# Performance work log

Hardware: AMD Instinct MI355X
Metric: run time of the kernel (lower is better)

Reference implementation:

```python
import jax, jax.numpy as jnp
import numpy as np
from jax import lax

VOCAB, D, H, K = 20000, 100, 100, 3
N_U, N_I, R, S, E = 256, 256, 8, 52, 20000


def _text_processor(reviews, emb_table, conv_w, conv_b):
    # reviews: [B,R,S] int -> c: [B,R,S',H]
    B, Rr, Ss = reviews.shape
    embs = emb_table[reviews]                              # [B,R,S,D]
    x = embs.reshape(B * Rr, 1, Ss, D)                     # NCHW
    c = lax.conv_general_dilated(x, conv_w, (1, 1), 'VALID',
                                 dimension_numbers=('NCHW', 'OIHW', 'NCHW'))
    c = jax.nn.relu(c + conv_b[None, :, None, None])       # [B*R,H,S',1]
    Sp = Ss - K + 1
    c = c[..., 0].transpose(0, 2, 1).reshape(B, Rr, Sp, H) # [B,R,S',H]
    return c


def _branch(reviews, emb_table, conv_w, conv_b, fc_w_w, fc_w_b, fc_w2_w, fc_w2_b):
    c = _text_processor(reviews, emb_table, conv_w, conv_b)
    rho = jax.nn.sigmoid(c @ fc_w_w.T + fc_w_b)            # [B,R,S',1]
    z = rho + lax.stop_gradient(jnp.round(rho) - rho)      # straight-through round
    z = z[..., 0]                                          # [B,R,S']
    P = jnp.max(c, axis=-2) @ fc_w2_w.T + fc_w2_b          # [B,R,D]
    return P, z


def reference(user_reviews, item_reviews, uid, iid, emb_table, conv_w, conv_b,
              fc_w_w, fc_w_b, fc_w2_w, fc_w2_b, h_r_w, h_c_w,
              user_bias, item_bias, global_bias):
    P_u, z_u = _branch(user_reviews, emb_table, conv_w, conv_b, fc_w_w, fc_w_b, fc_w2_w, fc_w2_b)
    P_i, z_i = _branch(item_reviews, emb_table, conv_w, conv_b, fc_w_w, fc_w_b, fc_w2_w, fc_w2_b)
    Pu, Pi = P_u[uid], P_i[iid]                            # edge gathers [E,R,D]
    zu, zi = z_u[uid], z_i[iid]                            # [E,R,S']
    s_uv = jnp.einsum('eud,evd->euv', Pu, Pi)              # per-edge review similarity [E,R,R]
    rho_u = jax.nn.sigmoid(s_uv.sum(-1))                   # [E,R]
    rho_v = jax.nn.sigmoid(s_uv.sum(-2))                   # [E,R]
    gamma_u_r = jnp.einsum('ers,er->es', zu, rho_u)        # [E,S']
    gamma_v_r = jnp.einsum('ers,er->es', zi, rho_v)
    pred_r = (jnp.concatenate([gamma_u_r, gamma_v_r], -1) @ h_r_w.T
              + user_bias[uid] + item_bias[iid] + global_bias)  # [E,1]
    gamma_u_c = jnp.einsum('er,erd->ed', rho_u, Pu)        # [E,D]
    gamma_v_c = jnp.einsum('er,erd->ed', rho_v, Pi)
    pred_c = jnp.concatenate([gamma_u_c, gamma_v_c], -1) @ h_c_w.T  # [E,1]
    return pred_r, pred_c, z_u, z_i


def setup_inputs() -> dict:
    key = jax.random.key(0)
    ks = jax.random.split(key, 12)
    return {
        'user_reviews': jax.random.randint(ks[0], (N_U, R, S), 0, VOCAB, dtype=jnp.int32),
        'item_reviews': jax.random.randint(ks[1], (N_I, R, S), 0, VOCAB, dtype=jnp.int32),
        'uid': jax.random.randint(ks[2], (E,), 0, N_U, dtype=jnp.int32),
        'iid': jax.random.randint(ks[3], (E,), 0, N_I, dtype=jnp.int32),
        'emb_table': jax.random.normal(ks[4], (VOCAB, D), jnp.float32) * 0.1,
        'conv_w': jax.random.normal(ks[5], (H, 1, K, D), jnp.float32) * 0.05,
        'conv_b': jnp.zeros((H,), jnp.float32),
        'fc_w_w': jax.random.normal(ks[6], (1, H), jnp.float32) * 0.1,
        'fc_w_b': jnp.zeros((1,), jnp.float32),
        'fc_w2_w': jax.random.normal(ks[7], (D, H), jnp.float32) * 0.1,
        'fc_w2_b': jnp.zeros((D,), jnp.float32),
        'h_r_w': jax.random.normal(ks[8], (1, 2 * (S - K + 1)), jnp.float32) * 0.1,
        'h_c_w': jax.random.normal(ks[9], (1, 2 * D), jnp.float32) * 0.1,
        'user_bias': jnp.zeros((N_U, 1), jnp.float32),
        'item_bias': jnp.zeros((N_I, 1), jnp.float32),
        'global_bias': jnp.zeros((1,), jnp.float32),
    }
```

## Files before the change

### kernel.cpp

```cpp
#include <hip/hip_runtime.h>
#include <math.h>


typedef __attribute__((ext_vector_type(8))) short short8;
typedef __attribute__((ext_vector_type(4))) float f32x4;

__device__ __forceinline__ float sigmoidf_(float x) { return 1.f / (1.f + expf(-x)); }
__device__ __forceinline__ ushort f2b(float f) {
    union { float f; unsigned int i; } c; c.f = f;
    unsigned int x = c.i;
    return (ushort)((x + 0x7fffu + ((x >> 16) & 1u)) >> 16);
}
__device__ __forceinline__ unsigned int pack_hl(float x) {
    union { float f; unsigned int i; } c; c.f = x;
    unsigned int hi = c.i & 0xFFFF0000u;
    union { float f; unsigned int i; } h; h.i = hi;
    return hi | (unsigned int)f2b(x - h.f);
}

#define Z_MARGIN 2e-3f
#define FLAG_CAP 204800

__global__ void k_prep(const float* __restrict__ conv_w, const float* __restrict__ fc_w2_w,
                       float* __restrict__ Wt, float* __restrict__ fc2t,
                       float* __restrict__ Psum, ushort* __restrict__ wpack,
                       int* __restrict__ flag_cnt) {
    int idx = blockIdx.x * 256 + threadIdx.x;
    if (idx < 30000) {
        int kk = idx / 100, h = idx - kk * 100;
        Wt[idx] = conv_w[h * 300 + kk];
    } else if (idx < 40000) {
        int j = idx - 30000;
        int h = j / 100, dd = j - h * 100;
        fc2t[j] = fc_w2_w[dd * 100 + h];
    } else if (idx < 91200) {
        Psum[idx - 40000] = 0.f;
    } else if (idx < 127040) {
        int j = idx - 91200;
        int frag = j >> 9, within = j & 511;
        int l = within >> 3, jj = within & 7;
        int kt = frag / 7, nt = frag % 7;
        int kk = kt * 32 + ((l >> 4) << 3) + jj;
        int h  = nt * 16 + (l & 15);
        ushort v = 0;
        if (kk < 300 && h < 100) v = f2b(conv_w[h * 300 + kk]);
        wpack[j] = v;
    } else if (idx == 127040) {
        *flag_cnt = 0;
    }
}

__global__ __launch_bounds__(256, 4)
void k_branch(const int* __restrict__ u_rev, const int* __restrict__ i_rev,
              const float* __restrict__ emb, const ushort* __restrict__ wpack,
              const float* __restrict__ conv_b, const float* __restrict__ fc_w_w,
              const float* __restrict__ fc_w_b, const float* __restrict__ fc_w2_b,
              const float* __restrict__ fc2t, const float* __restrict__ h_r_w,
              const float* __restrict__ h_c_w,
              float* __restrict__ Pbuf, float* __restrict__ Psum,
              float* __restrict__ zdot, float* __restrict__ Pdot,
              float* __restrict__ z_out, int* __restrict__ flag_cnt,
              int* __restrict__ flag_list) {
    __shared__ __align__(16) char smem[36816];
    unsigned int* xw   = (unsigned int*)smem;
    ushort* wbuf  = (ushort*)(smem + 26624);
    int*    s_tok = (int*)(smem + 33792);
    float*  s_vmax= (float*)(smem + 34000);
    float*  s_maxf= (float*)(smem + 35600);
    float*  s_z   = (float*)(smem + 36000);
    float*  s_lg  = (float*)(smem + 36208);
    float*  s_P   = (float*)(smem + 36416);

    const int tid = threadIdx.x, lane = tid & 63, w = tid >> 6;
    const int gi = blockIdx.x;
    const int branch = gi >> 11, inst = gi & 2047;

    const uint4* wp4 = (const uint4*)wpack;
    uint4* wbuf4 = (uint4*)wbuf;
    uint4 st0 = wp4[tid];
    uint4 st1; if (tid < 192) st1 = wp4[256 + tid];

    const int* rev = branch ? i_rev : u_rev;
    if (tid < 52) s_tok[tid] = rev[inst * 52 + tid];
    __syncthreads();

    {
        const float4* emb4 = (const float4*)emb;
        float4 v[6];
#pragma unroll
        for (int k = 0; k < 6; k++) {
            int idx = tid + (k << 8);
            if (idx < 1300) {
                int s = idx / 25, c = idx - s * 25;
                v[k] = emb4[s_tok[s] * 25 + c];
            }
        }
#pragma unroll
        for (int k = 0; k < 6; k++) {
            int idx = tid + (k << 8);
            if (idx < 1300) {
                uint4 o;
                o.x = pack_hl(v[k].x); o.y = pack_hl(v[k].y);
                o.z = pack_hl(v[k].z); o.w = pack_hl(v[k].w);
                *(uint4*)(xw + idx * 4) = o;
            }
        }
        for (int idx = 1300 + tid; idx < 1664; idx += 256) {
            uint4 z; z.x = 0u; z.y = 0u; z.z = 0u; z.w = 0u;
            *(uint4*)(xw + idx * 4) = z;
        }
    }

    wbuf4[tid] = st0;
    if (tid < 192) wbuf4[256 + tid] = st1;
    st0 = wp4[448 + tid];
    if (tid < 192) st1 = wp4[448 + 256 + tid];
    __syncthreads();

    f32x4 acc[7];
#pragma unroll
    for (int nt = 0; nt < 7; nt++) acc[nt] = (f32x4){0.f, 0.f, 0.f, 0.f};

    const int col = lane & 15, quad = lane >> 4, q8 = quad << 3;
    const int mt = w;

    for (int kt = 0; kt < 10; kt++) {
        {
            int e0 = (mt * 16 + col) * 100 + kt * 32 + q8;
            uint4 xa = *(const uint4*)(xw + e0);
            uint4 xb = *(const uint4*)(xw + e0 + 4);
            union AU { short8 s8; uint4 u; } ah, al;
            ah.u.x = (xa.x >> 16) | (xa.y & 0xFFFF0000u);
            ah.u.y = (xa.z >> 16) | (xa.w & 0xFFFF0000u);
            ah.u.z = (xb.x >> 16) | (xb.y & 0xFFFF0000u);
            ah.u.w = (xb.z >> 16) | (xb.w & 0xFFFF0000u);
            al.u.x = (xa.x & 0xFFFFu) | (xa.y << 16);
            al.u.y = (xa.z & 0xFFFFu) | (xa.w << 16);
            al.u.z = (xb.x & 0xFFFFu) | (xb.y << 16);
            al.u.w = (xb.z & 0xFFFFu) | (xb.w << 16);
#pragma unroll
            for (int nt = 0; nt < 7; nt++) {
                union BU { short8 s8; uint4 u4; } b;
                b.u4 = wbuf4[nt * 64 + lane];
                acc[nt] = __builtin_amdgcn_mfma_f32_16x16x32_bf16(al.s8, b.s8, acc[nt], 0, 0, 0);
                acc[nt] = __builtin_amdgcn_mfma_f32_16x16x32_bf16(ah.s8, b.s8, acc[nt], 0, 0, 0);
            }
        }
        __syncthreads();
        if (kt < 9) {
            wbuf4[tid] = st0;
            if (tid < 192) wbuf4[256 + tid] = st1;
            if (kt < 8) {
                st0 = wp4[(kt + 2) * 448 + tid];
                if (tid < 192) st1 = wp4[(kt + 2) * 448 + 256 + tid];
            }
            __syncthreads();
        }
    }

    float cb[7], fw[7], vmax[7];
#pragma unroll
    for (int nt = 0; nt < 7; nt++) {
        int h = nt * 16 + col;
        cb[nt] = (h < 100) ? conv_b[h] : 0.f;
        fw[nt] = (h < 100) ? fc_w_w[h] : 0.f;
        vmax[nt] = 0.f;
    }
    const float fcb = fc_w_b[0];

#pragma unroll
    for (int j = 0; j < 4; j++) {
        int p = mt * 16 + quad * 4 + j;
        bool pv = p < 50;
        float part = 0.f;
#pragma unroll
        for (int nt = 0; nt < 7; nt++) {
            float c = acc[nt][j] + cb[nt];
            c = c > 0.f ? c : 0.f;
            part += c * fw[nt];
            if (pv) vmax[nt] = fmaxf(vmax[nt], c);
        }
        part += __shfl_xor(part, 1, 64);
        part += __shfl_xor(part, 2, 64);
        part += __shfl_xor(part, 4, 64);
        part += __shfl_xor(part, 8, 64);
        if (pv && col == 0) {
            float logit = part + fcb;
            float z = rintf(sigmoidf_(logit));
            s_z[p] = z;
            s_lg[p] = logit;
            z_out[branch * 102400 + inst * 50 + p] = z;
        }
    }

#pragma unroll
    for (int nt = 0; nt < 7; nt++) {
        float m = vmax[nt];
        m = fmaxf(m, __shfl_xor(m, 16, 64));
        m = fmaxf(m, __shfl_xor(m, 32, 64));
        int h = nt * 16 + col;
        if (quad == 0 && h < 100) s_vmax[w * 100 + h] = m;
    }
    __syncthreads();

    if (tid < 100) {
        float mx = fmaxf(fmaxf(s_vmax[tid], s_vmax[100 + tid]),
                         fmaxf(s_vmax[200 + tid], s_vmax[300 + tid]));
        s_maxf[tid] = mx;
    }
    __syncthreads();

    if (tid < 100) {
        float a = fc_w2_b[tid];
        for (int h0 = 0; h0 < 100; h0 += 10) {
            float wv[10], mxv[10];
#pragma unroll
            for (int t = 0; t < 10; t++) {
                wv[t] = fc2t[(h0 + t) * 100 + tid];
                mxv[t] = s_maxf[h0 + t];
            }
#pragma unroll
            for (int t = 0; t < 10; t++) a += mxv[t] * wv[t];
        }
        Pbuf[gi * 100 + tid] = a;
        s_P[tid] = a;
        atomicAdd(&Psum[(branch * 256 + (inst >> 3)) * 100 + tid], a);
    }
    __syncthreads();

    if (w == 0) {
        float v = (lane < 50) ? s_z[lane] * h_r_w[branch * 50 + lane] : 0.f;
        for (int s = 1; s < 64; s <<= 1) v += __shfl_xor(v, s, 64);
        if (lane == 0) zdot[gi] = v;
    } else if (w == 1) {
        float u = 0.f;
        if (lane < 50) u = s_P[lane] * h_c_w[branch * 100 + lane]
                         + s_P[lane + 50] * h_c_w[branch * 100 + lane + 50];
        for (int s = 1; s < 64; s <<= 1) u += __shfl_xor(u, s, 64);
        if (lane == 0) Pdot[gi] = u;
    } else if (w == 2) {
        float lg = 1e9f;
        if (lane < 50) lg = s_lg[lane];
        unsigned long long mb = __ballot(fabsf(lg) < Z_MARGIN);
        int cnt = __popcll(mb);
        int base = 0;
        if (lane == 0 && cnt) base = atomicAdd(flag_cnt, cnt);
        base = __shfl(base, 0, 64);
        if (fabsf(lg) < Z_MARGIN) {
            int rank = __popcll(mb & ((1ull << lane) - 1ull));
            int k = base + rank;
            if (k < FLAG_CAP) flag_list[k] = gi * 50 + lane;
        }
    }
}

__launch_bounds__(256)
__global__ void k_refine(const int* __restrict__ u_rev, const int* __restrict__ i_rev,
                         const float* __restrict__ emb, const float* __restrict__ Wt,
                         const float* __restrict__ conv_b, const float* __restrict__ fc_w_w,
                         const float* __restrict__ fc_w_b, const float* __restrict__ h_r_w,
                         const int* __restrict__ flag_cnt, const int* __restrict__ flag_list,
                         float* __restrict__ z_out, float* __restrict__ zdot) {
    int n = *flag_cnt; if (n > FLAG_CAP) n = FLAG_CAP;
    const int lane = threadIdx.x & 63;
    const int wid = (blockIdx.x * 256 + threadIdx.x) >> 6;
    const int nw = gridDim.x * 4;
    const bool hv = lane < 50;
    const float cb0 = hv ? conv_b[lane] : 0.f;
    const float cb1 = hv ? conv_b[lane + 50] : 0.f;
    const float fw0 = hv ? fc_w_w[lane] : 0.f;
    const float fw1 = hv ? fc_w_w[lane + 50] : 0.f;
    const float fcb = fc_w_b[0];

    for (int e0 = wid * 4; e0 < n; e0 += nw * 4) {
        int gi[4], pos[4];
        bool iv[4];
        float xr[4][5];
#pragma unroll
        for (int m = 0; m < 4; m++) {
            int e = e0 + m;
            iv[m] = e < n;
            int code = iv[m] ? flag_list[e] : 0;
            gi[m] = code / 50; pos[m] = code - gi[m] * 50;
            const int* rev = (gi[m] >> 11) ? i_rev : u_rev;
            int tb = (gi[m] & 2047) * 52 + pos[m];
            int t0 = rev[tb], t1 = rev[tb + 1], t2 = rev[tb + 2];
#pragma unroll
            for (int s = 0; s < 5; s++) {
                int k = s * 64 + lane;
                float v = 0.f;
                if (k < 300) {
                    int r = k / 100, dd = k - r * 100;
                    int t = (r == 0) ? t0 : ((r == 1) ? t1 : t2);
                    v = emb[t * 100 + dd];
                }
                xr[m][s] = v;
            }
        }
        float c0[4], c1[4];
#pragma unroll
        for (int m = 0; m < 4; m++) { c0[m] = cb0; c1[m] = cb1; }
#pragma unroll
        for (int s = 0; s < 5; s++) {
            const int dmax = (s < 4) ? 64 : 44;
#pragma unroll 4
            for (int d2 = 0; d2 < dmax; d2++) {
                int d = s * 64 + d2;
                float w0 = hv ? Wt[d * 100 + lane] : 0.f;
                float w1 = hv ? Wt[d * 100 + lane + 50] : 0.f;
#pragma unroll
                for (int m = 0; m < 4; m++) {
                    float x = __shfl(xr[m][s], d2, 64);
                    c0[m] += x * w0;
                    c1[m] += x * w1;
                }
            }
        }
#pragma unroll
        for (int m = 0; m < 4; m++) {
            float v = fmaxf(c0[m], 0.f) * fw0 + fmaxf(c1[m], 0.f) * fw1;
            for (int s = 1; s < 64; s <<= 1) v += __shfl_xor(v, s, 64);
            if (lane == 0 && iv[m]) {
                int branch = gi[m] >> 11, inst = gi[m] & 2047;
                float z = rintf(sigmoidf_(v + fcb));
                float old = z_out[branch * 102400 + inst * 50 + pos[m]];
                if (z != old) {
                    z_out[branch * 102400 + inst * 50 + pos[m]] = z;
                    atomicAdd(&zdot[gi[m]], (z - old) * h_r_w[branch * 50 + pos[m]]);
                }
            }
        }
    }
}

__launch_bounds__(256)
__global__ void k_edge(const int* __restrict__ uid, const int* __restrict__ iid,
                       const float* __restrict__ Pbuf, const float* __restrict__ Psum,
                       const float* __restrict__ zdot, const float* __restrict__ Pdot,
                       const float* __restrict__ user_bias, const float* __restrict__ item_bias,
                       const float* __restrict__ global_bias, float* __restrict__ out) {
    int wave = threadIdx.x >> 6, lane = threadIdx.x & 63;
    int e = blockIdx.x * 4 + wave;
    int u = uid[e], i = iid[e];
    int g = lane >> 2, q = lane & 3;
    const float4* prow4; const float4* psum4; float wr, wc;
    if (g < 8) {
        prow4 = (const float4*)(Pbuf + (u * 8 + g) * 100);
        psum4 = (const float4*)(Psum + 25600 + i * 100);
        wr = zdot[u * 8 + g]; wc = Pdot[u * 8 + g];
    } else {
        prow4 = (const float4*)(Pbuf + (2048 + i * 8 + (g - 8)) * 100);
        psum4 = (const float4*)(Psum + u * 100);
        wr = zdot[2048 + i * 8 + (g - 8)]; wc = Pdot[2048 + i * 8 + (g - 8)];
    }
    float part = 0.f;
#pragma unroll
    for (int t = 0; t < 7; t++) {
        int c = q + 4 * t;
        if (c < 25) {
            float4 a = prow4[c], b = psum4[c];
            part += a.x * b.x + a.y * b.y + a.z * b.z + a.w * b.w;
        }
    }
    part += __shfl_xor(part, 1, 64);
    part += __shfl_xor(part, 2, 64);
    float sg = sigmoidf_(part);
    float cr = (q == 0) ? sg * wr : 0.f;
    float cc = (q == 0) ? sg * wc : 0.f;
    for (int s = 4; s < 64; s <<= 1) { cr += __shfl_xor(cr, s, 64); cc += __shfl_xor(cc, s, 64); }
    if (lane == 0) {
        out[e] = cr + user_bias[u] + item_bias[i] + global_bias[0];
        out[20000 + e] = cc;
    }
}

extern "C" void kernel_launch(void* const* d_in, const int* in_sizes, int n_in,
                              void* d_out, int out_size, void* d_ws, size_t ws_size,
                              hipStream_t stream) {
    const int*   u_rev    = (const int*)d_in[0];
    const int*   i_rev    = (const int*)d_in[1];
    const int*   uid      = (const int*)d_in[2];
    const int*   iid      = (const int*)d_in[3];
    const float* emb      = (const float*)d_in[4];
    const float* conv_w   = (const float*)d_in[5];
    const float* conv_b   = (const float*)d_in[6];
    const float* fc_w_w   = (const float*)d_in[7];
    const float* fc_w_b   = (const float*)d_in[8];
    const float* fc_w2_w  = (const float*)d_in[9];
    const float* fc_w2_b  = (const float*)d_in[10];
    const float* h_r_w    = (const float*)d_in[11];
    const float* h_c_w    = (const float*)d_in[12];
    const float* user_b   = (const float*)d_in[13];
    const float* item_b   = (const float*)d_in[14];
    const float* global_b = (const float*)d_in[15];
    float* out = (float*)d_out;

    float*  ws    = (float*)d_ws;
    float*  Pbuf  = ws;
    float*  Psum  = ws + 409600;
    float*  zdotb = ws + 460800;
    float*  Pdotb = ws + 464896;
    float*  Wt    = ws + 468992;
    float*  fc2t  = ws + 498992;
    ushort* wpack = (ushort*)(ws + 508992);
    int*    flagc = (int*)(ws + 526912);
    int*    flist = (int*)(ws + 526916);

    hipLaunchKernelGGL(k_prep, dim3(497), dim3(256), 0, stream,
                       conv_w, fc_w2_w, Wt, fc2t, Psum, wpack, flagc);
    hipLaunchKernelGGL(k_branch, dim3(4096), dim3(256), 0, stream,
                       u_rev, i_rev, emb, wpack, conv_b, fc_w_w, fc_w_b,
                       fc_w2_b, fc2t, h_r_w, h_c_w,
                       Pbuf, Psum, zdotb, Pdotb, out + 40000, flagc, flist);
    hipLaunchKernelGGL(k_refine, dim3(512), dim3(256), 0, stream,
                       u_rev, i_rev, emb, Wt, conv_b, fc_w_w, fc_w_b, h_r_w,
                       flagc, flist, out + 40000, zdotb);
    hipLaunchKernelGGL(k_edge, dim3(5000), dim3(256), 0, stream,
                       uid, iid, Pbuf, Psum, zdotb, Pdotb,
                       user_b, item_b, global_b, out);
}
```

Measured before the change: 211.6 us.

## Switch conv GEMM to single fp16 MFMA and precompute per-pair similarity matrix

Result: slower. 224.9 us (+6.3%).

```diff
diff --git a/kernel.cpp b/kernel.cpp
--- a/kernel.cpp
+++ b/kernel.cpp
@@ -1,30 +1,27 @@
 #include <hip/hip_runtime.h>
+#include <hip/hip_fp16.h>
 #include <math.h>
 
 
-typedef __attribute__((ext_vector_type(8))) short short8;
+typedef __attribute__((ext_vector_type(8))) _Float16 half8;
 typedef __attribute__((ext_vector_type(4))) float f32x4;
 
 __device__ __forceinline__ float sigmoidf_(float x) { return 1.f / (1.f + expf(-x)); }
-__device__ __forceinline__ ushort f2b(float f) {
-    union { float f; unsigned int i; } c; c.f = f;
-    unsigned int x = c.i;
-    return (ushort)((x + 0x7fffu + ((x >> 16) & 1u)) >> 16);
-}
-__device__ __forceinline__ unsigned int pack_hl(float x) {
-    union { float f; unsigned int i; } c; c.f = x;
-    unsigned int hi = c.i & 0xFFFF0000u;
-    union { float f; unsigned int i; } h; h.i = hi;
-    return hi | (unsigned int)f2b(x - h.f);
-}
-
-#define Z_MARGIN 2e-3f
+__device__ __forceinline__ ushort f2h(float x) {
+    union { __half h; ushort u; } t; t.h = __float2half(x); return t.u;
+}
+__device__ __forceinline__ float h2f(ushort u) {
+    union { __half h; ushort u; } t; t.u = u; return __half2float(t.h);
+}
+
+#define Z_MARGIN 4e-4f
 #define FLAG_CAP 204800
 
 __global__ void k_prep(const float* __restrict__ conv_w, const float* __restrict__ fc_w2_w,
+                       const float* __restrict__ emb,
                        float* __restrict__ Wt, float* __restrict__ fc2t,
                        float* __restrict__ Psum, ushort* __restrict__ wpack,
-                       int* __restrict__ flag_cnt) {
+                       int* __restrict__ flag_cnt, ushort* __restrict__ emb16) {
     int idx = blockIdx.x * 256 + threadIdx.x;
     if (idx < 30000) {
         int kk = idx / 100, h = idx - kk * 100;
@@ -42,17 +39,18 @@
         int kt = frag / 7, nt = frag % 7;
         int kk = kt * 32 + ((l >> 4) << 3) + jj;
         int h  = nt * 16 + (l & 15);
-        ushort v = 0;
-        if (kk < 300 && h < 100) v = f2b(conv_w[h * 300 + kk]);
-        wpack[j] = v;
+        wpack[j] = (kk < 300 && h < 100) ? f2h(conv_w[h * 300 + kk]) : (ushort)0;
     } else if (idx == 127040) {
         *flag_cnt = 0;
-    }
-}
-
-__global__ __launch_bounds__(256, 4)
+    } else {
+        int j = idx - 127041;
+        if (j < 2000000) emb16[j] = f2h(emb[j]);
+    }
+}
+
+__global__ __launch_bounds__(256, 6)
 void k_branch(const int* __restrict__ u_rev, const int* __restrict__ i_rev,
-              const float* __restrict__ emb, const ushort* __restrict__ wpack,
+              const ushort* __restrict__ emb16, const ushort* __restrict__ wpack,
               const float* __restrict__ conv_b, const float* __restrict__ fc_w_w,
               const float* __restrict__ fc_w_b, const float* __restrict__ fc_w2_b,
               const float* __restrict__ fc2t, const float* __restrict__ h_r_w,
@@ -61,15 +59,15 @@
               float* __restrict__ zdot, float* __restrict__ Pdot,
               float* __restrict__ z_out, int* __restrict__ flag_cnt,
               int* __restrict__ flag_list) {
-    __shared__ __align__(16) char smem[36816];
-    unsigned int* xw   = (unsigned int*)smem;
-    ushort* wbuf  = (ushort*)(smem + 26624);
-    int*    s_tok = (int*)(smem + 33792);
-    float*  s_vmax= (float*)(smem + 34000);
-    float*  s_maxf= (float*)(smem + 35600);
-    float*  s_z   = (float*)(smem + 36000);
-    float*  s_lg  = (float*)(smem + 36208);
-    float*  s_P   = (float*)(smem + 36416);
+    __shared__ __align__(16) char smem[23552];
+    ushort* xw    = (ushort*)smem;
+    ushort* wbuf  = (ushort*)(smem + 13312);
+    int*    s_tok = (int*)(smem + 20480);
+    float*  s_vmax= (float*)(smem + 20688);
+    float*  s_maxf= (float*)(smem + 22288);
+    float*  s_z   = (float*)(smem + 22688);
+    float*  s_lg  = (float*)(smem + 22896);
+    float*  s_P   = (float*)(smem + 23104);
 
     const int tid = threadIdx.x, lane = tid & 63, w = tid >> 6;
     const int gi = blockIdx.x;
@@ -85,30 +83,24 @@
     __syncthreads();
 
     {
-        const float4* emb4 = (const float4*)emb;
-        float4 v[6];
+        const uint2* emb2 = (const uint2*)emb16;
+        uint2 v[6];
 #pragma unroll
         for (int k = 0; k < 6; k++) {
             int idx = tid + (k << 8);
             if (idx < 1300) {
                 int s = idx / 25, c = idx - s * 25;
-                v[k] = emb4[s_tok[s] * 25 + c];
+                v[k] = emb2[s_tok[s] * 25 + c];
             }
         }
 #pragma unroll
         for (int k = 0; k < 6; k++) {
             int idx = tid + (k << 8);
-            if (idx < 1300) {
-                uint4 o;
-                o.x = pack_hl(v[k].x); o.y = pack_hl(v[k].y);
-                o.z = pack_hl(v[k].z); o.w = pack_hl(v[k].w);
-                *(uint4*)(xw + idx * 4) = o;
-            }
-        }
-        for (int idx = 1300 + tid; idx < 1664; idx += 256) {
-            uint4 z; z.x = 0u; z.y = 0u; z.z = 0u; z.w = 0u;
-            *(uint4*)(xw + idx * 4) = z;
-        }
+            if (idx < 1300) *(uint2*)(xw + idx * 4) = v[k];
+        }
+        uint4 z4; z4.x = 0u; z4.y = 0u; z4.z = 0u; z4.w = 0u;
+        for (int t2 = tid; t2 < 182; t2 += 256)
+            ((uint4*)xw)[650 + t2] = z4;
     }
 
     wbuf4[tid] = st0;
@@ -127,23 +119,14 @@
     for (int kt = 0; kt < 10; kt++) {
         {
             int e0 = (mt * 16 + col) * 100 + kt * 32 + q8;
-            uint4 xa = *(const uint4*)(xw + e0);
-            uint4 xb = *(const uint4*)(xw + e0 + 4);
-            union AU { short8 s8; uint4 u; } ah, al;
-            ah.u.x = (xa.x >> 16) | (xa.y & 0xFFFF0000u);
-            ah.u.y = (xa.z >> 16) | (xa.w & 0xFFFF0000u);
-            ah.u.z = (xb.x >> 16) | (xb.y & 0xFFFF0000u);
-            ah.u.w = (xb.z >> 16) | (xb.w & 0xFFFF0000u);
-            al.u.x = (xa.x & 0xFFFFu) | (xa.y << 16);
-            al.u.y = (xa.z & 0xFFFFu) | (xa.w << 16);
-            al.u.z = (xb.x & 0xFFFFu) | (xb.y << 16);
-            al.u.w = (xb.z & 0xFFFFu) | (xb.w << 16);
+            union AU { half8 h8; uint2 u2[2]; } a;
+            a.u2[0] = *(const uint2*)(xw + e0);
+            a.u2[1] = *(const uint2*)(xw + e0 + 4);
 #pragma unroll
             for (int nt = 0; nt < 7; nt++) {
-                union BU { short8 s8; uint4 u4; } b;
+                union BU { half8 h8; uint4 u4; } b;
                 b.u4 = wbuf4[nt * 64 + lane];
-                acc[nt] = __builtin_amdgcn_mfma_f32_16x16x32_bf16(al.s8, b.s8, acc[nt], 0, 0, 0);
-                acc[nt] = __builtin_amdgcn_mfma_f32_16x16x32_bf16(ah.s8, b.s8, acc[nt], 0, 0, 0);
+                acc[nt] = __builtin_amdgcn_mfma_f32_16x16x32_f16(a.h8, b.h8, acc[nt], 0, 0, 0);
             }
         }
         __syncthreads();
@@ -334,41 +317,60 @@
 }
 
 __launch_bounds__(256)
+__global__ void k_gmat(const float* __restrict__ Pbuf, const float* __restrict__ Psum,
+                       ushort* __restrict__ G) {
+    __shared__ __align__(16) float sv[100];
+    const int b = blockIdx.x, s = b >> 8, i = b & 255;
+    const int tid = threadIdx.x, lane = tid & 63, w = tid >> 6;
+    const float* vec = Psum + (s == 0 ? 25600 : 0) + i * 100;
+    if (tid < 100) sv[tid] = vec[tid];
+    __syncthreads();
+    const int g = lane >> 2, q = lane & 3;
+    const float4* rows4 = (const float4*)(Pbuf + s * 204800);
+    const float4* sv4 = (const float4*)sv;
+    for (int pass = 0; pass < 32; pass++) {
+        int j = pass * 64 + w * 16 + g;
+        float part = 0.f;
+#pragma unroll
+        for (int t = 0; t < 7; t++) {
+            int c = q + 4 * t;
+            if (c < 25) {
+                float4 a = rows4[j * 25 + c], bb = sv4[c];
+                part += a.x * bb.x + a.y * bb.y + a.z * bb.z + a.w * bb.w;
+            }
+        }
+        part += __shfl_xor(part, 1, 64);
+        part += __shfl_xor(part, 2, 64);
+        if (q == 0) G[s * 524288 + i * 2048 + j] = f2h(part);
+    }
+}
+
+__launch_bounds__(256)
 __global__ void k_edge(const int* __restrict__ uid, const int* __restrict__ iid,
-                       const float* __restrict__ Pbuf, const float* __restrict__ Psum,
+                       const ushort* __restrict__ G,
                        const float* __restrict__ zdot, const float* __restrict__ Pdot,
                        const float* __restrict__ user_bias, const float* __restrict__ item_bias,
                        const float* __restrict__ global_bias, float* __restrict__ out) {
-    int wave = threadIdx.x >> 6, lane = threadIdx.x & 63;
-    int e = blockIdx.x * 4 + wave;
+    const int tid = threadIdx.x, lane = tid & 63, w = tid >> 6;
+    const int e = blockIdx.x * 16 + w * 4 + (lane >> 4);
+    const int r = lane & 15;
     int u = uid[e], i = iid[e];
-    int g = lane >> 2, q = lane & 3;
-    const float4* prow4; const float4* psum4; float wr, wc;
-    if (g < 8) {
-        prow4 = (const float4*)(Pbuf + (u * 8 + g) * 100);
-        psum4 = (const float4*)(Psum + 25600 + i * 100);
-        wr = zdot[u * 8 + g]; wc = Pdot[u * 8 + g];
+    float gv, wr, wc;
+    if (r < 8) {
+        gv = h2f(G[i * 2048 + u * 8 + r]);
+        wr = zdot[u * 8 + r]; wc = Pdot[u * 8 + r];
     } else {
-        prow4 = (const float4*)(Pbuf + (2048 + i * 8 + (g - 8)) * 100);
-        psum4 = (const float4*)(Psum + u * 100);
-        wr = zdot[2048 + i * 8 + (g - 8)]; wc = Pdot[2048 + i * 8 + (g - 8)];
-    }
-    float part = 0.f;
-#pragma unroll
-    for (int t = 0; t < 7; t++) {
-        int c = q + 4 * t;
-        if (c < 25) {
-            float4 a = prow4[c], b = psum4[c];
-            part += a.x * b.x + a.y * b.y + a.z * b.z + a.w * b.w;
-        }
-    }
-    part += __shfl_xor(part, 1, 64);
-    part += __shfl_xor(part, 2, 64);
-    float sg = sigmoidf_(part);
-    float cr = (q == 0) ? sg * wr : 0.f;
-    float cc = (q == 0) ? sg * wc : 0.f;
-    for (int s = 4; s < 64; s <<= 1) { cr += __shfl_xor(cr, s, 64); cc += __shfl_xor(cc, s, 64); }
-    if (lane == 0) {
+        int a = r - 8;
+        gv = h2f(G[524288 + u * 2048 + i * 8 + a]);
+        wr = zdot[2048 + i * 8 + a]; wc = Pdot[2048 + i * 8 + a];
+    }
+    float sg = sigmoidf_(gv);
+    float cr = sg * wr, cc = sg * wc;
+    cr += __shfl_xor(cr, 1, 64); cc += __shfl_xor(cc, 1, 64);
+    cr += __shfl_xor(cr, 2, 64); cc += __shfl_xor(cc, 2, 64);
+    cr += __shfl_xor(cr, 4, 64); cc += __shfl_xor(cc, 4, 64);
+    cr += __shfl_xor(cr, 8, 64); cc += __shfl_xor(cc, 8, 64);
+    if (r == 0) {
         out[e] = cr + user_bias[u] + item_bias[i] + global_bias[0];
         out[20000 + e] = cc;
     }
@@ -405,17 +407,20 @@
     ushort* wpack = (ushort*)(ws + 508992);
     int*    flagc = (int*)(ws + 526912);
     int*    flist = (int*)(ws + 526916);
-
-    hipLaunchKernelGGL(k_prep, dim3(497), dim3(256), 0, stream,
-                       conv_w, fc_w2_w, Wt, fc2t, Psum, wpack, flagc);
+    ushort* emb16 = (ushort*)(ws + 731716);
+    ushort* Gbuf  = (ushort*)(ws + 1731716);
+
+    hipLaunchKernelGGL(k_prep, dim3(8309), dim3(256), 0, stream,
+                       conv_w, fc_w2_w, emb, Wt, fc2t, Psum, wpack, flagc, emb16);
     hipLaunchKernelGGL(k_branch, dim3(4096), dim3(256), 0, stream,
-                       u_rev, i_rev, emb, wpack, conv_b, fc_w_w, fc_w_b,
+                       u_rev, i_rev, emb16, wpack, conv_b, fc_w_w, fc_w_b,
                        fc_w2_b, fc2t, h_r_w, h_c_w,
                        Pbuf, Psum, zdotb, Pdotb, out + 40000, flagc, flist);
-    hipLaunchKernelGGL(k_refine, dim3(512), dim3(256), 0, stream,
+    hipLaunchKernelGGL(k_refine, dim3(128), dim3(256), 0, stream,
                        u_rev, i_rev, emb, Wt, conv_b, fc_w_w, fc_w_b, h_r_w,
                        flagc, flist, out + 40000, zdotb);
-    hipLaunchKernelGGL(k_edge, dim3(5000), dim3(256), 0, stream,
-                       uid, iid, Pbuf, Psum, zdotb, Pdotb,
+    hipLaunchKernelGGL(k_gmat, dim3(512), dim3(256), 0, stream, Pbuf, Psum, Gbuf);
+    hipLaunchKernelGGL(k_edge, dim3(1250), dim3(256), 0, stream,
+                       uid, iid, Gbuf, zdotb, Pdotb,
                        user_b, item_b, global_b, out);
 }
```
